# Kernel tuning notes

Measured on AMD Instinct MI355X. Metric: run time of the kernel, lower is better.

## Reference

```python
import jax, jax.numpy as jnp
import numpy as np

B, S_Q, S_KV = 4, 2048, 2048
D_MODEL, HEADS, D_QK, D_V = 1024, 16, 64, 64


def setup_inputs() -> dict:
    key = jax.random.key(0)
    ks = jax.random.split(key, 12)
    s = lambda fan_in: 1.0 / np.sqrt(fan_in)
    return {
        "x": jax.random.normal(ks[0], (B, S_Q, D_MODEL), jnp.float32),
        "encoder_output": jax.random.normal(ks[1], (B, S_KV, D_MODEL), jnp.float32),
        # per-head Linear weights stacked over heads: [H, D_MODEL, d_head]
        "Wq": jax.random.uniform(ks[2], (HEADS, D_MODEL, D_QK), jnp.float32, -s(D_MODEL), s(D_MODEL)),
        "bq": jax.random.uniform(ks[3], (HEADS, D_QK), jnp.float32, -s(D_MODEL), s(D_MODEL)),
        "Wk": jax.random.uniform(ks[4], (HEADS, D_MODEL, D_QK), jnp.float32, -s(D_MODEL), s(D_MODEL)),
        "bk": jax.random.uniform(ks[5], (HEADS, D_QK), jnp.float32, -s(D_MODEL), s(D_MODEL)),
        "Wv": jax.random.uniform(ks[6], (HEADS, D_MODEL, D_V), jnp.float32, -s(D_MODEL), s(D_MODEL)),
        "bv": jax.random.uniform(ks[7], (HEADS, D_V), jnp.float32, -s(D_MODEL), s(D_MODEL)),
        # output Linear: [H*D_V, D_MODEL]
        "Wo": jax.random.uniform(ks[8], (HEADS * D_V, D_MODEL), jnp.float32, -s(HEADS * D_V), s(HEADS * D_V)),
        "bo": jax.random.uniform(ks[9], (D_MODEL,), jnp.float32, -s(HEADS * D_V), s(HEADS * D_V)),
    }


def reference(x, encoder_output, Wq, bq, Wk, bk, Wv, bv, Wo, bo):
    # Batched equivalent of the per-head Python loop: project all heads at once.
    q = jnp.einsum("bqd,hde->bhqe", x, Wq) + bq[None, :, None, :]              # [B,H,Sq,dk]
    k = jnp.einsum("bsd,hde->bhse", encoder_output, Wk) + bk[None, :, None, :]  # [B,H,Skv,dk]
    v = jnp.einsum("bsd,hde->bhse", encoder_output, Wv) + bv[None, :, None, :]  # [B,H,Skv,dv]
    scale = 1.0 / jnp.sqrt(jnp.asarray(D_QK, x.dtype))
    scores = jnp.einsum("bhqe,bhse->bhqs", q, k) * scale                        # [B,H,Sq,Skv]
    attn = jax.nn.softmax(scores, axis=-1)
    heads = jnp.einsum("bhqs,bhse->bhqe", attn, v)                              # [B,H,Sq,dv]
    # concat heads on last dim (head order matches the torch list concat)
    multihead = heads.transpose(0, 2, 1, 3).reshape(x.shape[0], x.shape[1], HEADS * D_V)
    return multihead @ Wo + bo
```

## Files before the change

### kernel.cpp

```cpp
#include <hip/hip_runtime.h>
#include <hip/hip_bf16.h>
#include <stdint.h>

typedef unsigned short u16;
typedef __bf16 bf16x8 __attribute__((ext_vector_type(8)));
typedef float f32x4 __attribute__((ext_vector_type(4)));
typedef float f32x16 __attribute__((ext_vector_type(16)));
typedef unsigned short us8 __attribute__((ext_vector_type(8)));

__device__ __forceinline__ u16 f2bf(float f) {
  union { float f; uint32_t u; } v; v.f = f;
  uint32_t u = v.u;
  return (u16)((u + 0x7FFFu + ((u >> 16) & 1u)) >> 16);
}

__device__ __forceinline__ uint32_t cvtpk(float a, float b) {
  uint32_t r;
  asm("v_cvt_pk_bf16_f32 %0, %1, %2" : "=v"(r) : "v"(a), "v"(b));
  return r;
}

__device__ __forceinline__ void gload_lds16(const void* g, void* l) {
  __builtin_amdgcn_global_load_lds(
      (const __attribute__((address_space(1))) void*)(uintptr_t)g,
      (__attribute__((address_space(3))) void*)(uint32_t)(uintptr_t)l,
      16, 0, 0);
}

__device__ __forceinline__ float vsum16(f32x16 v) {
  float a = (v[0] + v[1]) + (v[2] + v[3]);
  float b = (v[4] + v[5]) + (v[6] + v[7]);
  float c = (v[8] + v[9]) + (v[10] + v[11]);
  float d = (v[12] + v[13]) + (v[14] + v[15]);
  return (a + b) + (c + d);
}

#define CROW(r, g) (((r) & 3) + 8 * ((r) >> 2) + 4 * (g))

__global__ __launch_bounds__(256) void cvt_all_k(
    const float* __restrict__ x, const float* __restrict__ enc,
    const float* __restrict__ Wq, const float* __restrict__ Wk,
    const float* __restrict__ Wv, const float* __restrict__ Wo,
    u16* __restrict__ xb, u16* __restrict__ eb,
    u16* __restrict__ wqb, u16* __restrict__ wkb,
    u16* __restrict__ wvb, u16* __restrict__ wob) {
  __shared__ float t[64][65];
  const int blk = blockIdx.x;
  const int tid = threadIdx.x;

  if (blk < 8192) {
    const float* in = (blk < 4096) ? x : enc;
    u16* out = (blk < 4096) ? xb : eb;
    size_t i = (size_t)(blk & 4095) * 256 + tid;
    const float4* p = (const float4*)in + i * 2;
    float4 a = p[0], b = p[1];
    us8 o;
    o[0] = f2bf(a.x); o[1] = f2bf(a.y); o[2] = f2bf(a.z); o[3] = f2bf(a.w);
    o[4] = f2bf(b.x); o[5] = f2bf(b.y); o[6] = f2bf(b.z); o[7] = f2bf(b.w);
    *(us8*)(out + i * 8) = o;
    return;
  }

  if (blk < 8960) {
    int r = blk - 8192;
    int z = r >> 8;
    const float* W = (z == 0) ? Wq : (z == 1) ? Wk : Wv;
    u16* o = (z == 0) ? wqb : (z == 1) ? wkb : wvb;
    const int h = (r & 255) >> 4, d0 = (r & 15) * 64;
    const float* Wb = W + ((size_t)h << 16) + (size_t)d0 * 64;
#pragma unroll
    for (int i = 0; i < 4; ++i) {
      int idx = tid + i * 256;
      int dl = idx >> 4, e4 = (idx & 15) << 2;
      float4 v = *(const float4*)(Wb + dl * 64 + e4);
      t[dl][e4 + 0] = v.x; t[dl][e4 + 1] = v.y; t[dl][e4 + 2] = v.z; t[dl][e4 + 3] = v.w;
    }
    __syncthreads();
#pragma unroll
    for (int i = 0; i < 2; ++i) {
      int idx = tid + i * 256;
      int e = idx >> 3, dc = (idx & 7) * 8;
      us8 w;
#pragma unroll
      for (int j = 0; j < 8; ++j) w[j] = f2bf(t[dc + j][e]);
      *(us8*)(o + ((size_t)(h * 64 + e)) * 1024 + d0 + dc) = w;
    }
    return;
  }

  {
    int r = blk - 8960;
    const int k0 = (r & 15) * 64, n0 = (r >> 4) * 64;
    const float* Wb = Wo + (size_t)k0 * 1024 + n0;
#pragma unroll
    for (int i = 0; i < 4; ++i) {
      int idx = tid + i * 256;
      int kl = idx >> 4, n4 = (idx & 15) << 2;
      float4 v = *(const float4*)(Wb + (size_t)kl * 1024 + n4);
      t[kl][n4 + 0] = v.x; t[kl][n4 + 1] = v.y; t[kl][n4 + 2] = v.z; t[kl][n4 + 3] = v.w;
    }
    __syncthreads();
#pragma unroll
    for (int i = 0; i < 2; ++i) {
      int idx = tid + i * 256;
      int n = idx >> 3, kc = (idx & 7) * 8;
      us8 w;
#pragma unroll
      for (int j = 0; j < 8; ++j) w[j] = f2bf(t[kc + j][n]);
      *(us8*)(wob + ((size_t)(n0 + n)) * 1024 + k0 + kc) = w;
    }
  }
}

__device__ __forceinline__ void gemm_core(const char* Ac, const char* Bc, int K,
                                          int m0, int n0, int tid,
                                          char* As0, char* As1, char* Bs0, char* Bs1,
                                          f32x4 (&acc)[4][4]) {
  const int wave = tid >> 6, lane = tid & 63;
  const int lo = lane & 15, hi = lane >> 4;
  const int wr = wave >> 1, wc = wave & 1;
  const int o0 = wave * 1024 + lane * 16;
  const int r0 = o0 >> 6, cb0 = o0 & 63;
  const int o1 = o0 + 4096;
  const int r1 = o1 >> 6, cb1 = o1 & 63;
  const size_t ksz = (size_t)K * 2;

  auto STAGE = [&](int t) {
    const size_t kb = (size_t)t * 64;
    char* Ad = (t & 1) ? As1 : As0;
    char* Bd = (t & 1) ? Bs1 : Bs0;
    gload_lds16(Ac + (size_t)(m0 + r0) * ksz + kb + cb0, Ad + o0);
    gload_lds16(Ac + (size_t)(m0 + r1) * ksz + kb + cb1, Ad + o1);
    gload_lds16(Bc + (size_t)(n0 + r0) * ksz + kb + cb0, Bd + o0);
    gload_lds16(Bc + (size_t)(n0 + r1) * ksz + kb + cb1, Bd + o1);
  };

  const int NK = K >> 5;
  STAGE(0);
  STAGE(1);

  for (int kk = 0; kk < NK; ++kk) {
    if (kk < NK - 1) {
      asm volatile("s_waitcnt vmcnt(4)" ::: "memory");
    } else {
      asm volatile("s_waitcnt vmcnt(0)" ::: "memory");
    }
    __builtin_amdgcn_s_barrier();
    __builtin_amdgcn_sched_barrier(0);
    const u16* Asb = (const u16*)((kk & 1) ? As1 : As0);
    const u16* Bsb = (const u16*)((kk & 1) ? Bs1 : Bs0);
    bf16x8 af[4], bfr[4];
#pragma unroll
    for (int i = 0; i < 4; ++i) {
      af[i]  = *(const bf16x8*)(Asb + (wr * 64 + i * 16 + lo) * 32 + hi * 8);
      bfr[i] = *(const bf16x8*)(Bsb + (wc * 64 + i * 16 + lo) * 32 + hi * 8);
    }
    asm volatile("s_waitcnt lgkmcnt(0)" ::: "memory");
    __builtin_amdgcn_sched_barrier(0);
    __builtin_amdgcn_s_barrier();
    if (kk + 2 < NK) STAGE(kk + 2);
    __builtin_amdgcn_s_setprio(1);
#pragma unroll
    for (int am = 0; am < 4; ++am)
#pragma unroll
      for (int bn = 0; bn < 4; ++bn)
        acc[am][bn] = __builtin_amdgcn_mfma_f32_16x16x32_bf16(af[am], bfr[bn], acc[am][bn], 0, 0, 0);
    __builtin_amdgcn_s_setprio(0);
  }
}

__global__ __launch_bounds__(256) void qkv_proj_k(
    const u16* __restrict__ xb, const u16* __restrict__ eb,
    const u16* __restrict__ wqb, const u16* __restrict__ wkvb,
    const float* __restrict__ bq, const float* __restrict__ bk_,
    const float* __restrict__ bv_,
    u16* __restrict__ Qg, u16* __restrict__ Kg, u16* __restrict__ Vt, float scale) {
  __shared__ __attribute__((aligned(16))) char As[2][8192];
  __shared__ __attribute__((aligned(16))) char Bs[2][8192];
  const int blk = blockIdx.x;
  const int tid = threadIdx.x;
  const int wave = tid >> 6, lane = tid & 63;
  const int lo = lane & 15, hi = lane >> 4;
  const int wr = wave >> 1, wc = wave & 1;

  f32x4 acc[4][4] = {};

  if (blk < 512) {
    const int n0 = (blk & 7) * 128, m0 = (blk >> 3) * 128;
    gemm_core((const char*)xb, (const char*)wqb, 1024, m0, n0, tid,
              As[0], As[1], Bs[0], Bs[1], acc);
#pragma unroll
    for (int bn = 0; bn < 4; ++bn) {
      int col = n0 + wc * 64 + bn * 16 + lo;
      float bb = bq[col];
      int hh = col >> 6, e = col & 63;
#pragma unroll
      for (int am = 0; am < 4; ++am) {
#pragma unroll
        for (int r = 0; r < 4; ++r) {
          int row = m0 + wr * 64 + am * 16 + hi * 4 + r;
          int b = row >> 11, s = row & 2047;
          Qg[(((size_t)(b * 16 + hh) * 2048 + s) << 6) + e] = f2bf((acc[am][bn][r] + bb) * scale);
        }
      }
    }
  } else {
    const int r_ = blk - 512;
    const int n0 = (r_ & 15) * 128, m0 = (r_ >> 4) * 128;
    gemm_core((const char*)eb, (const char*)wkvb, 1024, m0, n0, tid,
              As[0], As[1], Bs[0], Bs[1], acc);
    const bool isV = (n0 + wc * 64) >= 1024;
    if (!isV) {
#pragma unroll
      for (int bn = 0; bn < 4; ++bn) {
        int col = n0 + wc * 64 + bn * 16 + lo;
        float bb = bk_[col];
        int hh = col >> 6, e = col & 63;
#pragma unroll
        for (int am = 0; am < 4; ++am) {
#pragma unroll
          for (int r = 0; r < 4; ++r) {
            int row = m0 + wr * 64 + am * 16 + hi * 4 + r;
            int b = row >> 11, s = row & 2047;
            s = (s & ~12) | ((s & 4) << 1) | ((s & 8) >> 1);
            Kg[(((size_t)(b * 16 + hh) * 2048 + s) << 6) + e] = f2bf(acc[am][bn][r] + bb);
          }
        }
      }
    } else {
#pragma unroll
      for (int bn = 0; bn < 4; ++bn) {
        int c = (n0 + wc * 64 + bn * 16 + lo) - 1024;
        float bb = bv_[c];
        int hh = c >> 6, e = c & 63;
#pragma unroll
        for (int am = 0; am < 4; ++am) {
          int row = m0 + wr * 64 + am * 16 + hi * 4;
          int b = row >> 11, s = row & 2047;
          uint2 wv;
          wv.x = cvtpk(acc[am][bn][0] + bb, acc[am][bn][1] + bb);
          wv.y = cvtpk(acc[am][bn][2] + bb, acc[am][bn][3] + bb);
          *(uint2*)(Vt + (((size_t)(b * 16 + hh) * 64 + e) * 2048 + s)) = wv;
        }
      }
    }
  }
}

__global__ __launch_bounds__(256) void out_proj_k(const u16* __restrict__ A,
                                                  const u16* __restrict__ B,
                                                  const float* __restrict__ bias,
                                                  float* __restrict__ C, int M, int N, int K) {
  __shared__ __attribute__((aligned(16))) char As[2][8192];
  __shared__ __attribute__((aligned(16))) char Bs[2][8192];
  const int tid = threadIdx.x;
  const int wave = tid >> 6, lane = tid & 63;
  const int lo = lane & 15, hi = lane >> 4;
  const int wr = wave >> 1, wc = wave & 1;
  const int n0 = blockIdx.x * 128, m0 = blockIdx.y * 128;

  f32x4 acc[4][4] = {};
  gemm_core((const char*)A, (const char*)B, K, m0, n0, tid,
            As[0], As[1], Bs[0], Bs[1], acc);

#pragma unroll
  for (int bn = 0; bn < 4; ++bn) {
    int col = n0 + wc * 64 + bn * 16 + lo;
    float bb = bias[col];
#pragma unroll
    for (int am = 0; am < 4; ++am) {
#pragma unroll
      for (int r = 0; r < 4; ++r) {
        int row = m0 + wr * 64 + am * 16 + hi * 4 + r;
        C[(size_t)row * N + col] = acc[am][bn][r] + bb;
      }
    }
  }
}

__global__ __launch_bounds__(256, 3) void attn_k(const u16* __restrict__ Qg,
                                                 const u16* __restrict__ Kg,
                                                 const u16* __restrict__ Vtg,
                                                 u16* __restrict__ Hd) {
  const int W = blockIdx.x;
  const int bid = (W >> 7) * 128 + (W & 7) * 16 + ((W >> 3) & 15);
  const int bh = bid >> 4;
  const int q0 = (bid & 15) * 128;
  const int tid = threadIdx.x;
  const int w = tid >> 6, lane = tid & 63;
  const int q31 = lane & 31, g = lane >> 5;

  __shared__ __attribute__((aligned(16))) char LB[3][16384];

  bf16x8 qf0, qf1, qf2, qf3;
  {
    const char* Qrow = (const char*)(Qg + ((size_t)bh * 2048 + q0 + w * 32 + q31) * 64) + g * 16;
    qf0 = *(const bf16x8*)(Qrow);
    qf1 = *(const bf16x8*)(Qrow + 32);
    qf2 = *(const bf16x8*)(Qrow + 64);
    qf3 = *(const bf16x8*)(Qrow + 96);
  }

  f32x16 acc0 = {}, acc1 = {};
  float lrun = 0.f;

  const int lrow = lane >> 3;
  const int scol = ((lane & 7) ^ lrow) << 4;
  const char* kp = (const char*)Kg + (size_t)bh * 262144 + (size_t)(w * 16 + lrow) * 128 + scol;
  const char* vp = (const char*)Vtg + (size_t)bh * 262144 + (size_t)(w * 16 + lrow) * 4096 + scol;

  auto STAGE = [&](int c) {
    char* kb = &LB[c][0] + w * 2048;
    char* vb = kb + 8192;
    gload_lds16(kp, kb);
    gload_lds16(kp + 1024, kb + 1024);
    gload_lds16(vp, vb);
    gload_lds16(vp + 32768, vb + 1024);
    kp += 8192;
    vp += 128;
  };

  STAGE(0);
  STAGE(1);

  const int swz = (q31 & 7) << 4;
  const int krow = q31 * 128;
  const int ko0 = (g * 16) ^ swz;
  const int ko1 = (32 + g * 16) ^ swz;
  const int ko2 = (64 + g * 16) ^ swz;
  const int ko3 = (96 + g * 16) ^ swz;

  int bc = 0;
  for (int t = 0; t < 32; ++t) {
    if (t < 31) {
      asm volatile("s_waitcnt vmcnt(4)" ::: "memory");
    } else {
      asm volatile("s_waitcnt vmcnt(0)" ::: "memory");
    }
    __builtin_amdgcn_s_barrier();
    asm volatile("" ::: "memory");
    if (t < 30) STAGE(bc == 0 ? 2 : bc - 1);

    const char* Kc = &LB[bc][0];
    const char* Vc = Kc + 8192;

    f32x16 p0 = {}, p1 = {};
    __builtin_amdgcn_s_setprio(1);
    {
      bf16x8 kf;
      kf = *(const bf16x8*)(Kc + krow + ko0);
      p0 = __builtin_amdgcn_mfma_f32_32x32x16_bf16(kf, qf0, p0, 0, 0, 0);
      kf = *(const bf16x8*)(Kc + 4096 + krow + ko0);
      p1 = __builtin_amdgcn_mfma_f32_32x32x16_bf16(kf, qf0, p1, 0, 0, 0);
      kf = *(const bf16x8*)(Kc + krow + ko1);
      p0 = __builtin_amdgcn_mfma_f32_32x32x16_bf16(kf, qf1, p0, 0, 0, 0);
      kf = *(const bf16x8*)(Kc + 4096 + krow + ko1);
      p1 = __builtin_amdgcn_mfma_f32_32x32x16_bf16(kf, qf1, p1, 0, 0, 0);
      kf = *(const bf16x8*)(Kc + krow + ko2);
      p0 = __builtin_amdgcn_mfma_f32_32x32x16_bf16(kf, qf2, p0, 0, 0, 0);
      kf = *(const bf16x8*)(Kc + 4096 + krow + ko2);
      p1 = __builtin_amdgcn_mfma_f32_32x32x16_bf16(kf, qf2, p1, 0, 0, 0);
      kf = *(const bf16x8*)(Kc + krow + ko3);
      p0 = __builtin_amdgcn_mfma_f32_32x32x16_bf16(kf, qf3, p0, 0, 0, 0);
      kf = *(const bf16x8*)(Kc + 4096 + krow + ko3);
      p1 = __builtin_amdgcn_mfma_f32_32x32x16_bf16(kf, qf3, p1, 0, 0, 0);
    }
    __builtin_amdgcn_s_setprio(0);

#pragma unroll
    for (int i = 0; i < 16; ++i) p0[i] = __builtin_amdgcn_exp2f(p0[i]);
#pragma unroll
    for (int i = 0; i < 16; ++i) p1[i] = __builtin_amdgcn_exp2f(p1[i]);

    float rs = vsum16(p0) + vsum16(p1);
    {
      float ra = rs, rb = rs;
      asm("v_permlane32_swap_b32 %0, %1" : "+v"(ra), "+v"(rb));
      rs += g ? ra : rb;
    }
    lrun += rs;

    union PU { uint32_t u[4]; bf16x8 v; } a0, a1, a2, a3;
    a0.u[0] = cvtpk(p0[0], p0[1]);   a0.u[1] = cvtpk(p0[2], p0[3]);
    a0.u[2] = cvtpk(p0[4], p0[5]);   a0.u[3] = cvtpk(p0[6], p0[7]);
    a1.u[0] = cvtpk(p0[8], p0[9]);   a1.u[1] = cvtpk(p0[10], p0[11]);
    a1.u[2] = cvtpk(p0[12], p0[13]); a1.u[3] = cvtpk(p0[14], p0[15]);
    a2.u[0] = cvtpk(p1[0], p1[1]);   a2.u[1] = cvtpk(p1[2], p1[3]);
    a2.u[2] = cvtpk(p1[4], p1[5]);   a2.u[3] = cvtpk(p1[6], p1[7]);
    a3.u[0] = cvtpk(p1[8], p1[9]);   a3.u[1] = cvtpk(p1[10], p1[11]);
    a3.u[2] = cvtpk(p1[12], p1[13]); a3.u[3] = cvtpk(p1[14], p1[15]);

    __builtin_amdgcn_s_setprio(1);
    {
      bf16x8 vf;
      vf = *(const bf16x8*)(Vc + krow + ko0);
      acc0 = __builtin_amdgcn_mfma_f32_32x32x16_bf16(a0.v, vf, acc0, 0, 0, 0);
      vf = *(const bf16x8*)(Vc + 4096 + krow + ko0);
      acc1 = __builtin_amdgcn_mfma_f32_32x32x16_bf16(a0.v, vf, acc1, 0, 0, 0);
      vf = *(const bf16x8*)(Vc + krow + ko1);
      acc0 = __builtin_amdgcn_mfma_f32_32x32x16_bf16(a1.v, vf, acc0, 0, 0, 0);
      vf = *(const bf16x8*)(Vc + 4096 + krow + ko1);
      acc1 = __builtin_amdgcn_mfma_f32_32x32x16_bf16(a1.v, vf, acc1, 0, 0, 0);
      vf = *(const bf16x8*)(Vc + krow + ko2);
      acc0 = __builtin_amdgcn_mfma_f32_32x32x16_bf16(a2.v, vf, acc0, 0, 0, 0);
      vf = *(const bf16x8*)(Vc + 4096 + krow + ko2);
      acc1 = __builtin_amdgcn_mfma_f32_32x32x16_bf16(a2.v, vf, acc1, 0, 0, 0);
      vf = *(const bf16x8*)(Vc + krow + ko3);
      acc0 = __builtin_amdgcn_mfma_f32_32x32x16_bf16(a3.v, vf, acc0, 0, 0, 0);
      vf = *(const bf16x8*)(Vc + 4096 + krow + ko3);
      acc1 = __builtin_amdgcn_mfma_f32_32x32x16_bf16(a3.v, vf, acc1, 0, 0, 0);
    }
    __builtin_amdgcn_s_setprio(0);

    bc = (bc == 2) ? 0 : bc + 1;
  }

  float linv = 1.f / lrun;
  const int b = bh >> 4, h = bh & 15;
  u16* Ho = Hd + ((size_t)b * 2048 + q0 + w * 32) * 1024 + h * 64;
#pragma unroll
  for (int r = 0; r < 16; ++r) {
    float iv = __shfl(linv, CROW(r, g));
    int q = CROW(r, g);
    u16* row = Ho + (size_t)q * 1024;
    row[q31]      = f2bf(acc0[r] * iv);
    row[32 + q31] = f2bf(acc1[r] * iv);
  }
}


extern "C" void kernel_launch(void* const* d_in, const int* in_sizes, int n_in,
                              void* d_out, int out_size, void* d_ws, size_t ws_size,
                              hipStream_t stream) {
  const float* x   = (const float*)d_in[0];
  const float* enc = (const float*)d_in[1];
  const float* Wq  = (const float*)d_in[2];
  const float* bq  = (const float*)d_in[3];
  const float* Wk  = (const float*)d_in[4];
  const float* bk  = (const float*)d_in[5];
  const float* Wv  = (const float*)d_in[6];
  const float* bv  = (const float*)d_in[7];
  const float* Wo  = (const float*)d_in[8];
  const float* bo  = (const float*)d_in[9];
  float* out = (float*)d_out;
  char* ws = (char*)d_ws;

  const size_t SZ = 16u * 1024u * 1024u;
  u16* xb  = (u16*)(ws + 0 * SZ);
  u16* eb  = (u16*)(ws + 1 * SZ);
  u16* Qg  = (u16*)(ws + 2 * SZ);
  u16* Kg  = (u16*)(ws + 3 * SZ);
  u16* vtb = (u16*)(ws + 4 * SZ);
  u16* wqb = (u16*)(ws + 5 * SZ + 0u * (2u << 20));
  u16* wkb = (u16*)(ws + 5 * SZ + 1u * (2u << 20));
  u16* wob = (u16*)(ws + 5 * SZ + 3u * (2u << 20));
  u16* hd  = xb;

  const float cs = 0.18033688011112042f;

  cvt_all_k<<<9216, 256, 0, stream>>>(x, enc, Wq, Wk, Wv, Wo, xb, eb, wqb, wkb,
                                      (u16*)(ws + 5 * SZ + 2u * (2u << 20)), wob);

  qkv_proj_k<<<1536, 256, 0, stream>>>(xb, eb, wqb, wkb, bq, bk, bv, Qg, Kg, vtb, cs);

  attn_k<<<1024, 256, 0, stream>>>(Qg, Kg, vtb, hd);

  out_proj_k<<<dim3(8, 64), 256, 0, stream>>>(hd, wob, bo, out, 8192, 1024, 1024);
}
```

Baseline: 193.6 us.

## Process two query tiles per attention block to reuse each K/V stage

Each attention block now handles 256 query rows instead of 128, running two independent 128-row tiles against every staged K/V chunk. This halves K/V global traffic and the block count, and moves from triple buffering with a partial vmcnt wait to double buffering with a full wait before each barrier. The block-to-work remap also changes. In exchange, register pressure rises because of the extra Q fragments and accumulators, and the launch-bounds occupancy hint is dropped. Only 512 blocks remain, and the load/compute overlap is shallower.

```diff
diff --git a/kernel.cpp b/kernel.cpp
--- a/kernel.cpp
+++ b/kernel.cpp
@@ -278,31 +278,36 @@
   }
 }
 
-__global__ __launch_bounds__(256, 3) void attn_k(const u16* __restrict__ Qg,
-                                                 const u16* __restrict__ Kg,
-                                                 const u16* __restrict__ Vtg,
-                                                 u16* __restrict__ Hd) {
+__global__ __launch_bounds__(256) void attn_k(const u16* __restrict__ Qg,
+                                              const u16* __restrict__ Kg,
+                                              const u16* __restrict__ Vtg,
+                                              u16* __restrict__ Hd) {
   const int W = blockIdx.x;
-  const int bid = (W >> 7) * 128 + (W & 7) * 16 + ((W >> 3) & 15);
-  const int bh = bid >> 4;
-  const int q0 = (bid & 15) * 128;
+  const int bid = (W & 7) * 64 + (W >> 3);
+  const int bh = bid >> 3;
+  const int q0 = (bid & 7) * 256;
   const int tid = threadIdx.x;
   const int w = tid >> 6, lane = tid & 63;
   const int q31 = lane & 31, g = lane >> 5;
 
-  __shared__ __attribute__((aligned(16))) char LB[3][16384];
-
-  bf16x8 qf0, qf1, qf2, qf3;
+  __shared__ __attribute__((aligned(16))) char LB[2][16384];
+
+  bf16x8 qa0, qa1, qa2, qa3, qb0, qb1, qb2, qb3;
   {
-    const char* Qrow = (const char*)(Qg + ((size_t)bh * 2048 + q0 + w * 32 + q31) * 64) + g * 16;
-    qf0 = *(const bf16x8*)(Qrow);
-    qf1 = *(const bf16x8*)(Qrow + 32);
-    qf2 = *(const bf16x8*)(Qrow + 64);
-    qf3 = *(const bf16x8*)(Qrow + 96);
-  }
-
-  f32x16 acc0 = {}, acc1 = {};
-  float lrun = 0.f;
+    const char* QrA = (const char*)(Qg + ((size_t)bh * 2048 + q0 + w * 32 + q31) * 64) + g * 16;
+    qa0 = *(const bf16x8*)(QrA);
+    qa1 = *(const bf16x8*)(QrA + 32);
+    qa2 = *(const bf16x8*)(QrA + 64);
+    qa3 = *(const bf16x8*)(QrA + 96);
+    const char* QrB = QrA + 16384;
+    qb0 = *(const bf16x8*)(QrB);
+    qb1 = *(const bf16x8*)(QrB + 32);
+    qb2 = *(const bf16x8*)(QrB + 64);
+    qb3 = *(const bf16x8*)(QrB + 96);
+  }
+
+  f32x16 accA0 = {}, accA1 = {}, accB0 = {}, accB1 = {};
+  float lrunA = 0.f, lrunB = 0.f;
 
   const int lrow = lane >> 3;
   const int scol = ((lane & 7) ^ lrow) << 4;
@@ -321,7 +326,6 @@
   };
 
   STAGE(0);
-  STAGE(1);
 
   const int swz = (q31 & 7) << 4;
   const int krow = q31 * 128;
@@ -330,40 +334,28 @@
   const int ko2 = (64 + g * 16) ^ swz;
   const int ko3 = (96 + g * 16) ^ swz;
 
-  int bc = 0;
-  for (int t = 0; t < 32; ++t) {
-    if (t < 31) {
-      asm volatile("s_waitcnt vmcnt(4)" ::: "memory");
-    } else {
-      asm volatile("s_waitcnt vmcnt(0)" ::: "memory");
-    }
-    __builtin_amdgcn_s_barrier();
-    asm volatile("" ::: "memory");
-    if (t < 30) STAGE(bc == 0 ? 2 : bc - 1);
-
-    const char* Kc = &LB[bc][0];
-    const char* Vc = Kc + 8192;
-
+  auto TILE = [&](const char* Kc, const char* Vc, bf16x8 f0, bf16x8 f1, bf16x8 f2,
+                  bf16x8 f3, f32x16& o0, f32x16& o1, float& lr) {
     f32x16 p0 = {}, p1 = {};
     __builtin_amdgcn_s_setprio(1);
     {
       bf16x8 kf;
       kf = *(const bf16x8*)(Kc + krow + ko0);
-      p0 = __builtin_amdgcn_mfma_f32_32x32x16_bf16(kf, qf0, p0, 0, 0, 0);
+      p0 = __builtin_amdgcn_mfma_f32_32x32x16_bf16(kf, f0, p0, 0, 0, 0);
       kf = *(const bf16x8*)(Kc + 4096 + krow + ko0);
-      p1 = __builtin_amdgcn_mfma_f32_32x32x16_bf16(kf, qf0, p1, 0, 0, 0);
+      p1 = __builtin_amdgcn_mfma_f32_32x32x16_bf16(kf, f0, p1, 0, 0, 0);
       kf = *(const bf16x8*)(Kc + krow + ko1);
-      p0 = __builtin_amdgcn_mfma_f32_32x32x16_bf16(kf, qf1, p0, 0, 0, 0);
+      p0 = __builtin_amdgcn_mfma_f32_32x32x16_bf16(kf, f1, p0, 0, 0, 0);
       kf = *(const bf16x8*)(Kc + 4096 + krow + ko1);
-      p1 = __builtin_amdgcn_mfma_f32_32x32x16_bf16(kf, qf1, p1, 0, 0, 0);
+      p1 = __builtin_amdgcn_mfma_f32_32x32x16_bf16(kf, f1, p1, 0, 0, 0);
       kf = *(const bf16x8*)(Kc + krow + ko2);
-      p0 = __builtin_amdgcn_mfma_f32_32x32x16_bf16(kf, qf2, p0, 0, 0, 0);
+      p0 = __builtin_amdgcn_mfma_f32_32x32x16_bf16(kf, f2, p0, 0, 0, 0);
       kf = *(const bf16x8*)(Kc + 4096 + krow + ko2);
-      p1 = __builtin_amdgcn_mfma_f32_32x32x16_bf16(kf, qf2, p1, 0, 0, 0);
+      p1 = __builtin_amdgcn_mfma_f32_32x32x16_bf16(kf, f2, p1, 0, 0, 0);
       kf = *(const bf16x8*)(Kc + krow + ko3);
-      p0 = __builtin_amdgcn_mfma_f32_32x32x16_bf16(kf, qf3, p0, 0, 0, 0);
+      p0 = __builtin_amdgcn_mfma_f32_32x32x16_bf16(kf, f3, p0, 0, 0, 0);
       kf = *(const bf16x8*)(Kc + 4096 + krow + ko3);
-      p1 = __builtin_amdgcn_mfma_f32_32x32x16_bf16(kf, qf3, p1, 0, 0, 0);
+      p1 = __builtin_amdgcn_mfma_f32_32x32x16_bf16(kf, f3, p1, 0, 0, 0);
     }
     __builtin_amdgcn_s_setprio(0);
 
@@ -378,7 +370,7 @@
       asm("v_permlane32_swap_b32 %0, %1" : "+v"(ra), "+v"(rb));
       rs += g ? ra : rb;
     }
-    lrun += rs;
+    lr += rs;
 
     union PU { uint32_t u[4]; bf16x8 v; } a0, a1, a2, a3;
     a0.u[0] = cvtpk(p0[0], p0[1]);   a0.u[1] = cvtpk(p0[2], p0[3]);
@@ -394,37 +386,65 @@
     {
       bf16x8 vf;
       vf = *(const bf16x8*)(Vc + krow + ko0);
-      acc0 = __builtin_amdgcn_mfma_f32_32x32x16_bf16(a0.v, vf, acc0, 0, 0, 0);
+      o0 = __builtin_amdgcn_mfma_f32_32x32x16_bf16(a0.v, vf, o0, 0, 0, 0);
       vf = *(const bf16x8*)(Vc + 4096 + krow + ko0);
-      acc1 = __builtin_amdgcn_mfma_f32_32x32x16_bf16(a0.v, vf, acc1, 0, 0, 0);
+      o1 = __builtin_amdgcn_mfma_f32_32x32x16_bf16(a0.v, vf, o1, 0, 0, 0);
       vf = *(const bf16x8*)(Vc + krow + ko1);
-      acc0 = __builtin_amdgcn_mfma_f32_32x32x16_bf16(a1.v, vf, acc0, 0, 0, 0);
+      o0 = __builtin_amdgcn_mfma_f32_32x32x16_bf16(a1.v, vf, o0, 0, 0, 0);
       vf = *(const bf16x8*)(Vc + 4096 + krow + ko1);
-      acc1 = __builtin_amdgcn_mfma_f32_32x32x16_bf16(a1.v, vf, acc1, 0, 0, 0);
+      o1 = __builtin_amdgcn_mfma_f32_32x32x16_bf16(a1.v, vf, o1, 0, 0, 0);
       vf = *(const bf16x8*)(Vc + krow + ko2);
-      acc0 = __builtin_amdgcn_mfma_f32_32x32x16_bf16(a2.v, vf, acc0, 0, 0, 0);
+      o0 = __builtin_amdgcn_mfma_f32_32x32x16_bf16(a2.v, vf, o0, 0, 0, 0);
       vf = *(const bf16x8*)(Vc + 4096 + krow + ko2);
-      acc1 = __builtin_amdgcn_mfma_f32_32x32x16_bf16(a2.v, vf, acc1, 0, 0, 0);
+      o1 = __builtin_amdgcn_mfma_f32_32x32x16_bf16(a2.v, vf, o1, 0, 0, 0);
       vf = *(const bf16x8*)(Vc + krow + ko3);
-      acc0 = __builtin_amdgcn_mfma_f32_32x32x16_bf16(a3.v, vf, acc0, 0, 0, 0);
+      o0 = __builtin_amdgcn_mfma_f32_32x32x16_bf16(a3.v, vf, o0, 0, 0, 0);
       vf = *(const bf16x8*)(Vc + 4096 + krow + ko3);
-      acc1 = __builtin_amdgcn_mfma_f32_32x32x16_bf16(a3.v, vf, acc1, 0, 0, 0);
+      o1 = __builtin_amdgcn_mfma_f32_32x32x16_bf16(a3.v, vf, o1, 0, 0, 0);
     }
     __builtin_amdgcn_s_setprio(0);
-
-    bc = (bc == 2) ? 0 : bc + 1;
-  }
-
-  float linv = 1.f / lrun;
+  };
+
+  int cur = 0;
+  for (int t = 0; t < 32; ++t) {
+    asm volatile("s_waitcnt vmcnt(0)" ::: "memory");
+    __builtin_amdgcn_s_barrier();
+    asm volatile("" ::: "memory");
+    if (t < 31) STAGE(cur ^ 1);
+
+    const char* Kc = &LB[cur][0];
+    const char* Vc = Kc + 8192;
+
+    TILE(Kc, Vc, qa0, qa1, qa2, qa3, accA0, accA1, lrunA);
+    TILE(Kc, Vc, qb0, qb1, qb2, qb3, accB0, accB1, lrunB);
+
+    cur ^= 1;
+  }
+
   const int b = bh >> 4, h = bh & 15;
-  u16* Ho = Hd + ((size_t)b * 2048 + q0 + w * 32) * 1024 + h * 64;
-#pragma unroll
-  for (int r = 0; r < 16; ++r) {
-    float iv = __shfl(linv, CROW(r, g));
-    int q = CROW(r, g);
-    u16* row = Ho + (size_t)q * 1024;
-    row[q31]      = f2bf(acc0[r] * iv);
-    row[32 + q31] = f2bf(acc1[r] * iv);
+  {
+    float linv = 1.f / lrunA;
+    u16* Ho = Hd + ((size_t)b * 2048 + q0 + w * 32) * 1024 + h * 64;
+#pragma unroll
+    for (int r = 0; r < 16; ++r) {
+      float iv = __shfl(linv, CROW(r, g));
+      int q = CROW(r, g);
+      u16* row = Ho + (size_t)q * 1024;
+      row[q31]      = f2bf(accA0[r] * iv);
+      row[32 + q31] = f2bf(accA1[r] * iv);
+    }
+  }
+  {
+    float linv = 1.f / lrunB;
+    u16* Ho = Hd + ((size_t)b * 2048 + q0 + 128 + w * 32) * 1024 + h * 64;
+#pragma unroll
+    for (int r = 0; r < 16; ++r) {
+      float iv = __shfl(linv, CROW(r, g));
+      int q = CROW(r, g);
+      u16* row = Ho + (size_t)q * 1024;
+      row[q31]      = f2bf(accB0[r] * iv);
+      row[32 + q31] = f2bf(accB1[r] * iv);
+    }
   }
 }
 
@@ -463,7 +483,7 @@
 
   qkv_proj_k<<<1536, 256, 0, stream>>>(xb, eb, wqb, wkb, bq, bk, bv, Qg, Kg, vtb, cs);
 
-  attn_k<<<1024, 256, 0, stream>>>(Qg, Kg, vtb, hd);
+  attn_k<<<512, 256, 0, stream>>>(Qg, Kg, vtb, hd);
 
   out_proj_k<<<dim3(8, 64), 256, 0, stream>>>(hd, wob, bo, out, 8192, 1024, 1024);
 }
```

Measured after the change: 199.7 us. 3.1% more time.

## Compute softmax row sums via MFMA with ones vector and double-buffer LDS

Applied to the files above, without the earlier changes.

Replaces the per-iteration VALU row-sum reduction and cross-lane permlane swap with an extra MFMA that multiplies the bf16 probabilities by a ones vector, accumulating row sums in a separate accumulator that already sits in the output row layout. The triple-buffered LDS ring becomes a double buffer with a full vmcnt(0) wait each iteration, and the launch bound is raised to 4 blocks per CU. This lowers LDS use and VALU work to allow higher occupancy, at the cost of 25% more MFMA work in the PV stage, less prefetch depth, and row sums computed from bf16-rounded probabilities.

```diff
diff --git a/kernel.cpp b/kernel.cpp
--- a/kernel.cpp
+++ b/kernel.cpp
@@ -25,14 +25,6 @@
       (const __attribute__((address_space(1))) void*)(uintptr_t)g,
       (__attribute__((address_space(3))) void*)(uint32_t)(uintptr_t)l,
       16, 0, 0);
-}
-
-__device__ __forceinline__ float vsum16(f32x16 v) {
-  float a = (v[0] + v[1]) + (v[2] + v[3]);
-  float b = (v[4] + v[5]) + (v[6] + v[7]);
-  float c = (v[8] + v[9]) + (v[10] + v[11]);
-  float d = (v[12] + v[13]) + (v[14] + v[15]);
-  return (a + b) + (c + d);
 }
 
 #define CROW(r, g) (((r) & 3) + 8 * ((r) >> 2) + 4 * (g))
@@ -278,7 +270,7 @@
   }
 }
 
-__global__ __launch_bounds__(256, 3) void attn_k(const u16* __restrict__ Qg,
+__global__ __launch_bounds__(256, 4) void attn_k(const u16* __restrict__ Qg,
                                                  const u16* __restrict__ Kg,
                                                  const u16* __restrict__ Vtg,
                                                  u16* __restrict__ Hd) {
@@ -290,7 +282,7 @@
   const int w = tid >> 6, lane = tid & 63;
   const int q31 = lane & 31, g = lane >> 5;
 
-  __shared__ __attribute__((aligned(16))) char LB[3][16384];
+  __shared__ __attribute__((aligned(16))) char LB[2][16384];
 
   bf16x8 qf0, qf1, qf2, qf3;
   {
@@ -301,8 +293,10 @@
     qf3 = *(const bf16x8*)(Qrow + 96);
   }
 
-  f32x16 acc0 = {}, acc1 = {};
-  float lrun = 0.f;
+  union { uint32_t u[4]; bf16x8 v; } ones;
+  ones.u[0] = ones.u[1] = ones.u[2] = ones.u[3] = 0x3F803F80u;
+
+  f32x16 acc0 = {}, acc1 = {}, accL = {};
 
   const int lrow = lane >> 3;
   const int scol = ((lane & 7) ^ lrow) << 4;
@@ -321,7 +315,6 @@
   };
 
   STAGE(0);
-  STAGE(1);
 
   const int swz = (q31 & 7) << 4;
   const int krow = q31 * 128;
@@ -330,18 +323,14 @@
   const int ko2 = (64 + g * 16) ^ swz;
   const int ko3 = (96 + g * 16) ^ swz;
 
-  int bc = 0;
+  int cur = 0;
   for (int t = 0; t < 32; ++t) {
-    if (t < 31) {
-      asm volatile("s_waitcnt vmcnt(4)" ::: "memory");
-    } else {
-      asm volatile("s_waitcnt vmcnt(0)" ::: "memory");
-    }
+    asm volatile("s_waitcnt vmcnt(0)" ::: "memory");
     __builtin_amdgcn_s_barrier();
     asm volatile("" ::: "memory");
-    if (t < 30) STAGE(bc == 0 ? 2 : bc - 1);
-
-    const char* Kc = &LB[bc][0];
+    if (t < 31) STAGE(cur ^ 1);
+
+    const char* Kc = &LB[cur][0];
     const char* Vc = Kc + 8192;
 
     f32x16 p0 = {}, p1 = {};
@@ -372,14 +361,6 @@
 #pragma unroll
     for (int i = 0; i < 16; ++i) p1[i] = __builtin_amdgcn_exp2f(p1[i]);
 
-    float rs = vsum16(p0) + vsum16(p1);
-    {
-      float ra = rs, rb = rs;
-      asm("v_permlane32_swap_b32 %0, %1" : "+v"(ra), "+v"(rb));
-      rs += g ? ra : rb;
-    }
-    lrun += rs;
-
     union PU { uint32_t u[4]; bf16x8 v; } a0, a1, a2, a3;
     a0.u[0] = cvtpk(p0[0], p0[1]);   a0.u[1] = cvtpk(p0[2], p0[3]);
     a0.u[2] = cvtpk(p0[4], p0[5]);   a0.u[3] = cvtpk(p0[6], p0[7]);
@@ -397,30 +378,33 @@
       acc0 = __builtin_amdgcn_mfma_f32_32x32x16_bf16(a0.v, vf, acc0, 0, 0, 0);
       vf = *(const bf16x8*)(Vc + 4096 + krow + ko0);
       acc1 = __builtin_amdgcn_mfma_f32_32x32x16_bf16(a0.v, vf, acc1, 0, 0, 0);
+      accL = __builtin_amdgcn_mfma_f32_32x32x16_bf16(a0.v, ones.v, accL, 0, 0, 0);
       vf = *(const bf16x8*)(Vc + krow + ko1);
       acc0 = __builtin_amdgcn_mfma_f32_32x32x16_bf16(a1.v, vf, acc0, 0, 0, 0);
       vf = *(const bf16x8*)(Vc + 4096 + krow + ko1);
       acc1 = __builtin_amdgcn_mfma_f32_32x32x16_bf16(a1.v, vf, acc1, 0, 0, 0);
+      accL = __builtin_amdgcn_mfma_f32_32x32x16_bf16(a1.v, ones.v, accL, 0, 0, 0);
       vf = *(const bf16x8*)(Vc + krow + ko2);
       acc0 = __builtin_amdgcn_mfma_f32_32x32x16_bf16(a2.v, vf, acc0, 0, 0, 0);
       vf = *(const bf16x8*)(Vc + 4096 + krow + ko2);
       acc1 = __builtin_amdgcn_mfma_f32_32x32x16_bf16(a2.v, vf, acc1, 0, 0, 0);
+      accL = __builtin_amdgcn_mfma_f32_32x32x16_bf16(a2.v, ones.v, accL, 0, 0, 0);
       vf = *(const bf16x8*)(Vc + krow + ko3);
       acc0 = __builtin_amdgcn_mfma_f32_32x32x16_bf16(a3.v, vf, acc0, 0, 0, 0);
       vf = *(const bf16x8*)(Vc + 4096 + krow + ko3);
       acc1 = __builtin_amdgcn_mfma_f32_32x32x16_bf16(a3.v, vf, acc1, 0, 0, 0);
+      accL = __builtin_amdgcn_mfma_f32_32x32x16_bf16(a3.v, ones.v, accL, 0, 0, 0);
     }
     __builtin_amdgcn_s_setprio(0);
 
-    bc = (bc == 2) ? 0 : bc + 1;
-  }
-
-  float linv = 1.f / lrun;
+    cur ^= 1;
+  }
+
   const int b = bh >> 4, h = bh & 15;
   u16* Ho = Hd + ((size_t)b * 2048 + q0 + w * 32) * 1024 + h * 64;
 #pragma unroll
   for (int r = 0; r < 16; ++r) {
-    float iv = __shfl(linv, CROW(r, g));
+    float iv = __builtin_amdgcn_rcpf(accL[r]);
     int q = CROW(r, g);
     u16* row = Ho + (size_t)q * 1024;
     row[q31]      = f2bf(acc0[r] * iv);
```

Measured after the change: 197.8 us. 2.1% more time.
